# Kernel tuning notes

Measured on AMD Instinct MI355X. Metric: run time of the kernel, lower is better.

## Reference

```python
import jax, jax.numpy as jnp
import numpy as np

B, T, D, H = 4, 2048, 1024, 16
Dh = D // H

def setup_inputs() -> dict:
    key = jax.random.key(0)
    ks = jax.random.split(key, 6)
    scale = 1.0 / np.sqrt(D)
    return {
        "x": jax.random.normal(ks[0], (B, T, D), dtype=jnp.float32),
        "W_q": jax.random.normal(ks[1], (D, D), dtype=jnp.float32) * scale,
        "W_k": jax.random.normal(ks[2], (D, D), dtype=jnp.float32) * scale,
        "W_v": jax.random.normal(ks[3], (D, D), dtype=jnp.float32) * scale,
        "W_o": jax.random.normal(ks[4], (D, D), dtype=jnp.float32) * scale,
        "b_o": jax.random.normal(ks[5], (D,), dtype=jnp.float32) * 0.02,
    }

def reference(x, W_q, W_k, W_v, W_o, b_o):
    # Linear weights stored torch-style (out, in): y = x @ W.T
    def split_heads(z):
        return z.reshape(B, T, H, Dh).transpose(0, 2, 1, 3)  # [B,H,T,Dh]
    q = split_heads(x @ W_q.T)
    k = split_heads(x @ W_k.T)
    v = split_heads(x @ W_v.T)
    scale = Dh ** -0.5
    attn = jnp.einsum('bhqd,bhkd->bhqk', q, k) * scale  # [B,H,T,T]
    causal = jnp.tril(jnp.ones((T, T), dtype=bool))
    attn = jnp.where(causal[None, None], attn, -jnp.inf)
    attn = jax.nn.softmax(attn, axis=-1)
    y = jnp.einsum('bhqk,bhkd->bhqd', attn, v)  # [B,H,T,Dh]
    y = y.transpose(0, 2, 1, 3).reshape(B, T, D)
    return y @ W_o.T + b_o
```

## Files before the change

kernel.cpp:

```cpp
#include <hip/hip_runtime.h>
#include <hip/hip_bf16.h>
#include <stdint.h>

#define B_   4
#define T_   2048
#define H_   16
#define MTOT (B_ * T_)
#define NQKV 3072
#define QSC  0.18033688f

typedef __attribute__((ext_vector_type(8))) __bf16 bf16x8;
typedef __attribute__((ext_vector_type(4))) float f32x4;
typedef __attribute__((ext_vector_type(16))) float f32x16;
typedef __attribute__((ext_vector_type(4))) float f4v;
typedef __attribute__((ext_vector_type(4))) unsigned short us4;
typedef __attribute__((ext_vector_type(8))) unsigned short us8;
typedef __attribute__((ext_vector_type(4))) unsigned int u32x4;

static __device__ __forceinline__ unsigned short f2bf(float f) {
  __hip_bfloat16 h = __float2bfloat16(f);
  return __builtin_bit_cast(unsigned short, h);
}

static __device__ __forceinline__ float fast_exp2(float x) {
#if __has_builtin(__builtin_amdgcn_exp2f)
  return __builtin_amdgcn_exp2f(x);
#else
  float r; asm("v_exp_f32 %0, %1" : "=v"(r) : "v"(x)); return r;
#endif
}

static __device__ __forceinline__ void async16(const void* g, void* l) {
  __builtin_amdgcn_global_load_lds(
      (const __attribute__((address_space(1))) void*)g,
      (__attribute__((address_space(3))) void*)l, 16, 0, 0);
}

#define XHALF(res, x, OP)                                  \
  {                                                        \
    float t1_ = (x), t2_ = (x);                            \
    asm("" : "+v"(t2_));                                   \
    asm("v_permlane32_swap_b32 %0, %1" : "+v"(t1_), "+v"(t2_)); \
    res = OP(t1_, t2_);                                    \
  }
static __device__ __forceinline__ float fadd_(float a, float b) { return a + b; }

__global__ __launch_bounds__(256) void cvt_all(
    const float* __restrict__ x, const float* __restrict__ Wq,
    const float* __restrict__ Wk, const float* __restrict__ Wv,
    const float* __restrict__ Wo, unsigned short* __restrict__ xb,
    unsigned short* __restrict__ wqkv, unsigned short* __restrict__ wo) {
  int i = blockIdx.x * blockDim.x + threadIdx.x;
  const float* s; unsigned short* d; int j;
  if (i < 2097152)      { s = x;  d = xb;             j = i; }
  else if (i < 2359296) { s = Wq; d = wqkv;           j = i - 2097152; }
  else if (i < 2621440) { s = Wk; d = wqkv + 1048576; j = i - 2359296; }
  else if (i < 2883584) { s = Wv; d = wqkv + 2097152; j = i - 2621440; }
  else                  { s = Wo; d = wo;             j = i - 2883584; }
  f4v v = reinterpret_cast<const f4v*>(s)[j];
  us4 o;
  o.x = f2bf(v.x); o.y = f2bf(v.y); o.z = f2bf(v.z); o.w = f2bf(v.w);
  reinterpret_cast<us4*>(d)[j] = o;
}

template <int MODE>
__global__ __launch_bounds__(256) void gemm_bt(
    const unsigned short* __restrict__ A,
    const unsigned short* __restrict__ Bw,
    unsigned short* __restrict__ Cb,
    float* __restrict__ Cf,
    const float* __restrict__ bias,
    int K, int N) {
  __shared__ __align__(16) unsigned short As[128 * 32];
  __shared__ __align__(16) unsigned short Bs[128 * 32];

  const int t = threadIdx.x;
  const int lane = t & 63;
  const int w = t >> 6;
  const int lr = lane & 15;
  const int lg = lane >> 4;
  const int wm = w >> 1;
  const int wn = w & 1;
  const int m0 = blockIdx.y * 128;
  const int n0 = blockIdx.x * 128;

  f32x4 acc[4][4];
#pragma unroll
  for (int i = 0; i < 4; ++i)
#pragma unroll
    for (int j = 0; j < 4; ++j) acc[i][j] = (f32x4){0.f, 0.f, 0.f, 0.f};

  const int srow = t >> 2;
  const int scol = (t & 3) * 8;
  const unsigned short* ga = A + (size_t)(m0 + srow) * K + scol;
  const unsigned short* gb = Bw + (size_t)(n0 + srow) * K + scol;

  for (int k0 = 0; k0 < K; k0 += 32) {
    async16(ga + k0,                  &As[t * 8]);
    async16(ga + k0 + (size_t)64 * K, &As[2048 + t * 8]);
    async16(gb + k0,                  &Bs[t * 8]);
    async16(gb + k0 + (size_t)64 * K, &Bs[2048 + t * 8]);
    __syncthreads();

    bf16x8 af[4], bfr[4];
#pragma unroll
    for (int mi = 0; mi < 4; ++mi)
      af[mi] = *(const bf16x8*)&As[(wm * 64 + mi * 16 + lr) * 32 + lg * 8];
#pragma unroll
    for (int ni = 0; ni < 4; ++ni)
      bfr[ni] = *(const bf16x8*)&Bs[(wn * 64 + ni * 16 + lr) * 32 + lg * 8];
#pragma unroll
    for (int mi = 0; mi < 4; ++mi)
#pragma unroll
      for (int ni = 0; ni < 4; ++ni)
        acc[mi][ni] = __builtin_amdgcn_mfma_f32_16x16x32_bf16(
            af[mi], bfr[ni], acc[mi][ni], 0, 0, 0);
    __syncthreads();
  }

#pragma unroll
  for (int mi = 0; mi < 4; ++mi) {
    const int row = m0 + wm * 64 + mi * 16 + lg * 4;
#pragma unroll
    for (int ni = 0; ni < 4; ++ni) {
      const int col = n0 + wn * 64 + ni * 16 + lr;
#pragma unroll
      for (int r = 0; r < 4; ++r) {
        if (MODE == 1) {
          Cf[(size_t)(row + r) * N + col] = acc[mi][ni][r] + bias[col];
        } else {
          float v = acc[mi][ni][r];
          if (col < 1024) v *= QSC;
          Cb[(size_t)(row + r) * N + col] = f2bf(v);
        }
      }
    }
  }
}

__global__ __launch_bounds__(256, 4) void attn_kernel(
    const unsigned short* __restrict__ qkv, unsigned short* __restrict__ ob) {
  const int bid = blockIdx.x;
  const int pair = bid & 63;
  const int g = bid >> 6;
  const int rnd = g >> 2, idx = g & 3;
  const int qg = (rnd == 0) ? (15 - idx)
               : (rnd == 1) ? (8 + idx)
               : (rnd == 2) ? (7 - idx) : idx;
  const int b = pair >> 4;
  const int h = pair & 15;
  const int t = threadIdx.x;
  const int w = t >> 6;
  const int lane = t & 63;
  const int l31 = lane & 31;
  const int hi = lane >> 5;

  const int q0w = qg * 128 + w * 32;
  const int myBound = 2 * qg + (w >> 1);
  const int NT = 2 * qg + 2;

  __shared__ __align__(16) unsigned short Ks[2][64 * 64];
  __shared__ __align__(16) unsigned short Vs[2][64 * 64];

  const size_t rowbase = (size_t)(b * T_) * NQKV;

  bf16x8 Qf[4];
  {
    const unsigned short* qp =
        qkv + rowbase + (size_t)(q0w + l31) * NQKV + h * 64 + hi * 8;
#pragma unroll
    for (int m = 0; m < 4; ++m) Qf[m] = *(const bf16x8*)(qp + m * 16);
  }

  const int kr = t >> 3;
  const int ks = t & 7;
  const unsigned short* kbase =
      qkv + rowbase + 1024 + h * 64 + (ks ^ (kr & 7)) * 8 + (size_t)kr * NQKV;
  const int kvr = t >> 2;
  const int dc2 = (t & 3) * 2;
  const unsigned short* vbase =
      qkv + rowbase + 2048 + h * 64 + dc2 * 8 + (size_t)kvr * NQKV;

  float m_i = -INFINITY, l_i = 0.f;
  f32x16 o[2];
#pragma unroll
  for (int r = 0; r < 16; ++r) { o[0][r] = 0.f; o[1][r] = 0.f; }

#define VSCATTER(Vb, v0, v1)                                       \
  {                                                                \
    _Pragma("unroll") for (int i = 0; i < 8; ++i) {                \
      const int s0 = ((kvr >> 3) ^ dc2 ^ i) & 7;                   \
      const int s1 = ((kvr >> 3) ^ (dc2 + 1) ^ i) & 7;             \
      (Vb)[(dc2 * 8 + i) * 64 + s0 * 8 + (kvr & 7)] = (v0)[i];     \
      (Vb)[((dc2 + 1) * 8 + i) * 64 + s1 * 8 + (kvr & 7)] = (v1)[i]; \
    }                                                              \
  }

  {
    async16(kbase, &Ks[0][t * 8]);
    async16(kbase + (size_t)32 * NQKV, &Ks[0][2048 + t * 8]);
    us8 v0 = *(const us8*)vbase;
    us8 v1 = *(const us8*)(vbase + 8);
    VSCATTER(&Vs[0][0], v0, v1);
  }

  int cur = 0;
  for (int kt = 0; kt < NT; ++kt) {
    __syncthreads();

    const bool pf = (kt + 1 < NT);
    us8 v0, v1;
    if (pf) {
      const size_t off = (size_t)(kt + 1) * 64 * NQKV;
      async16(kbase + off, &Ks[cur ^ 1][t * 8]);
      async16(kbase + off + (size_t)32 * NQKV, &Ks[cur ^ 1][2048 + t * 8]);
      v0 = *(const us8*)(vbase + off);
      v1 = *(const us8*)(vbase + off + 8);
    }

    if (kt <= myBound) {
      const unsigned short* Kb = Ks[cur];
      const unsigned short* Vb = Vs[cur];

      f32x16 a0, a1;
#pragma unroll
      for (int r = 0; r < 16; ++r) { a0[r] = 0.f; a1[r] = 0.f; }
      {
        const int rb0 = l31 * 64;
        const int rb1 = (32 + l31) * 64;
        const int r7 = l31 & 7;
        __builtin_amdgcn_s_setprio(1);
#pragma unroll
        for (int m = 0; m < 4; ++m) {
          const int c = (((m << 1) | hi) ^ r7) * 8;
          bf16x8 kf0 = *(const bf16x8*)&Kb[rb0 + c];
          bf16x8 kf1 = *(const bf16x8*)&Kb[rb1 + c];
          a0 = __builtin_amdgcn_mfma_f32_32x32x16_bf16(kf0, Qf[m], a0, 0, 0, 0);
          a1 = __builtin_amdgcn_mfma_f32_32x32x16_bf16(kf1, Qf[m], a1, 0, 0, 0);
        }
        __builtin_amdgcn_s_setprio(0);
      }

      if (kt == myBound) {
        const int qglob = q0w + l31;
#pragma unroll
        for (int r = 0; r < 16; ++r) {
          const int kvb = kt * 64 + (r & 3) + ((r >> 2) << 3) + (hi << 2);
          if (kvb > qglob) a0[r] = -INFINITY;
          if (kvb + 32 > qglob) a1[r] = -INFINITY;
        }
      }

      float m8[8];
#pragma unroll
      for (int j = 0; j < 8; ++j)
        m8[j] = fmaxf(fmaxf(a0[j], a0[j + 8]), fmaxf(a1[j], a1[j + 8]));
      float pp = fmaxf(fmaxf(fmaxf(m8[0], m8[4]), fmaxf(m8[1], m8[5])),
                       fmaxf(fmaxf(m8[2], m8[6]), fmaxf(m8[3], m8[7])));
      float pmax;
      XHALF(pmax, pp, fmaxf);
      if (__any(pmax > m_i + 8.f)) {
        const float mnew = fmaxf(m_i, pmax);
        const float al = fast_exp2(m_i - mnew);
        m_i = mnew;
        l_i *= al;
#pragma unroll
        for (int r = 0; r < 16; ++r) { o[0][r] *= al; o[1][r] *= al; }
      }

#pragma unroll
      for (int r = 0; r < 16; ++r) {
        a0[r] = fast_exp2(a0[r] - m_i);
        a1[r] = fast_exp2(a1[r] - m_i);
      }
      float s8[8];
#pragma unroll
      for (int j = 0; j < 8; ++j)
        s8[j] = (a0[j] + a0[j + 8]) + (a1[j] + a1[j + 8]);
      float rp = ((s8[0] + s8[1]) + (s8[2] + s8[3])) +
                 ((s8[4] + s8[5]) + (s8[6] + s8[7]));
      float rs;
      XHALF(rs, rp, fadd_);
      l_i += rs;

      bf16x8 Pf[4];
#pragma unroll
      for (int m = 0; m < 4; ++m) {
        const int rb2 = (m & 1) * 8;
        uint32_t u0, u1, u2, u3;
        const f32x16& s = (m >> 1) ? a1 : a0;
        asm("v_cvt_pk_bf16_f32 %0, %1, %2" : "=v"(u0) : "v"(s[rb2 + 0]), "v"(s[rb2 + 1]));
        asm("v_cvt_pk_bf16_f32 %0, %1, %2" : "=v"(u1) : "v"(s[rb2 + 2]), "v"(s[rb2 + 3]));
        asm("v_cvt_pk_bf16_f32 %0, %1, %2" : "=v"(u2) : "v"(s[rb2 + 4]), "v"(s[rb2 + 5]));
        asm("v_cvt_pk_bf16_f32 %0, %1, %2" : "=v"(u3) : "v"(s[rb2 + 6]), "v"(s[rb2 + 7]));
        asm("v_permlane32_swap_b32 %0, %1" : "+v"(u0), "+v"(u2));
        asm("v_permlane32_swap_b32 %0, %1" : "+v"(u1), "+v"(u3));
        u32x4 pw = {u0, u1, u2, u3};
        Pf[m] = __builtin_bit_cast(bf16x8, pw);
      }

      __builtin_amdgcn_s_setprio(1);
#pragma unroll
      for (int dt = 0; dt < 2; ++dt) {
        const int d = dt * 32 + l31;
        const int base = d * 64;
        const int dsw = ((d >> 3) ^ d) & 7;
#pragma unroll
        for (int m = 0; m < 4; ++m) {
          bf16x8 vf = *(const bf16x8*)&Vb[base + ((((m << 1) | hi) ^ dsw) & 7) * 8];
          o[dt] = __builtin_amdgcn_mfma_f32_32x32x16_bf16(vf, Pf[m], o[dt], 0, 0, 0);
        }
      }
      __builtin_amdgcn_s_setprio(0);
    }

    if (pf) VSCATTER(&Vs[cur ^ 1][0], v0, v1);
    cur ^= 1;
  }

  const float rl = 1.0f / l_i;
#pragma unroll
  for (int dt = 0; dt < 2; ++dt) {
    float s[16];
#pragma unroll
    for (int r = 0; r < 16; ++r) s[r] = o[dt][r] * rl;
    uint32_t u[8];
#pragma unroll
    for (int p = 0; p < 8; ++p)
      asm("v_cvt_pk_bf16_f32 %0, %1, %2" : "=v"(u[p]) : "v"(s[2 * p]), "v"(s[2 * p + 1]));
    asm("v_permlane32_swap_b32 %0, %1" : "+v"(u[0]), "+v"(u[2]));
    asm("v_permlane32_swap_b32 %0, %1" : "+v"(u[1]), "+v"(u[3]));
    asm("v_permlane32_swap_b32 %0, %1" : "+v"(u[4]), "+v"(u[6]));
    asm("v_permlane32_swap_b32 %0, %1" : "+v"(u[5]), "+v"(u[7]));
    unsigned short* op =
        ob + (size_t)(b * T_ + q0w + l31) * 1024 + h * 64 + dt * 32 + hi * 8;
    u32x4 c0 = {u[0], u[1], u[2], u[3]};
    u32x4 c1 = {u[4], u[5], u[6], u[7]};
    *(u32x4*)op = c0;
    *(u32x4*)(op + 16) = c1;
  }
}

extern "C" void kernel_launch(void* const* d_in, const int* in_sizes, int n_in,
                              void* d_out, int out_size, void* d_ws,
                              size_t ws_size, hipStream_t stream) {
  const float* x = (const float*)d_in[0];
  const float* Wq = (const float*)d_in[1];
  const float* Wk = (const float*)d_in[2];
  const float* Wv = (const float*)d_in[3];
  const float* Wo = (const float*)d_in[4];
  const float* bo = (const float*)d_in[5];
  float* out = (float*)d_out;

  char* ws = (char*)d_ws;
  unsigned short* xb   = (unsigned short*)(ws + 0);
  unsigned short* wqkv = (unsigned short*)(ws + 16777216);
  unsigned short* wo   = (unsigned short*)(ws + 23068672);
  unsigned short* qkv  = (unsigned short*)(ws + 25165824);
  unsigned short* ob   = (unsigned short*)(ws + 75497472);
  if (ws_size < 92274688u) return;

  cvt_all<<<12288, 256, 0, stream>>>(x, Wq, Wk, Wv, Wo, xb, wqkv, wo);

  gemm_bt<0><<<dim3(NQKV / 128, MTOT / 128), 256, 0, stream>>>(
      xb, wqkv, qkv, nullptr, nullptr, 1024, NQKV);

  attn_kernel<<<dim3(1024), 256, 0, stream>>>(qkv, ob);

  gemm_bt<1><<<dim3(1024 / 128, MTOT / 128), 256, 0, stream>>>(
      ob, wo, nullptr, out, bo, 1024, 1024);
}
```

Before: 184.4 us.

## Widen GEMM K-tile to 64 with XOR-swizzled LDS and XCD-aware block mapping

The GEMM kernel now stages 64-wide K slices per iteration, which halves the number of barrier pairs. Its shared-memory layout is XOR-swizzled to avoid bank conflicts on the fragment reads. Blocks are remapped from a 1D grid so that each XCD (chosen by blockIdx & 7) gets a contiguous band of M rows, to improve L2 reuse of the A tiles. Doubling the LDS footprint may lower occupancy, and the load stage is still not overlapped with compute.

```diff
diff --git a/kernel.cpp b/kernel.cpp
--- a/kernel.cpp
+++ b/kernel.cpp
@@ -63,7 +63,7 @@
   reinterpret_cast<us4*>(d)[j] = o;
 }
 
-template <int MODE>
+template <int MODE, int NT>
 __global__ __launch_bounds__(256) void gemm_bt(
     const unsigned short* __restrict__ A,
     const unsigned short* __restrict__ Bw,
@@ -71,8 +71,14 @@
     float* __restrict__ Cf,
     const float* __restrict__ bias,
     int K, int N) {
-  __shared__ __align__(16) unsigned short As[128 * 32];
-  __shared__ __align__(16) unsigned short Bs[128 * 32];
+  __shared__ __align__(16) unsigned short As[128 * 64];
+  __shared__ __align__(16) unsigned short Bs[128 * 64];
+
+  const int bid = blockIdx.x;
+  const int xcd = bid & 7;
+  const int loc = bid >> 3;
+  const int m0 = (xcd * 8 + loc / NT) * 128;
+  const int n0 = (loc % NT) * 128;
 
   const int t = threadIdx.x;
   const int lane = t & 63;
@@ -81,8 +87,6 @@
   const int lg = lane >> 4;
   const int wm = w >> 1;
   const int wn = w & 1;
-  const int m0 = blockIdx.y * 128;
-  const int n0 = blockIdx.x * 128;
 
   f32x4 acc[4][4];
 #pragma unroll
@@ -90,31 +94,38 @@
 #pragma unroll
     for (int j = 0; j < 4; ++j) acc[i][j] = (f32x4){0.f, 0.f, 0.f, 0.f};
 
-  const int srow = t >> 2;
-  const int scol = (t & 3) * 8;
-  const unsigned short* ga = A + (size_t)(m0 + srow) * K + scol;
-  const unsigned short* gb = Bw + (size_t)(n0 + srow) * K + scol;
-
-  for (int k0 = 0; k0 < K; k0 += 32) {
-    async16(ga + k0,                  &As[t * 8]);
-    async16(ga + k0 + (size_t)64 * K, &As[2048 + t * 8]);
-    async16(gb + k0,                  &Bs[t * 8]);
-    async16(gb + k0 + (size_t)64 * K, &Bs[2048 + t * 8]);
+  const int srow = t >> 3;
+  const int gs = (t & 7) ^ ((t >> 3) & 7);
+  const unsigned short* ga = A + (size_t)(m0 + srow) * K + gs * 8;
+  const unsigned short* gb = Bw + (size_t)(n0 + srow) * K + gs * 8;
+
+  const int rsw = lr & 7;
+
+  for (int k0 = 0; k0 < K; k0 += 64) {
+#pragma unroll
+    for (int k = 0; k < 4; ++k) {
+      async16(ga + (size_t)(k * 32) * K + k0, &As[(k * 256 + t) * 8]);
+      async16(gb + (size_t)(k * 32) * K + k0, &Bs[(k * 256 + t) * 8]);
+    }
     __syncthreads();
 
-    bf16x8 af[4], bfr[4];
-#pragma unroll
-    for (int mi = 0; mi < 4; ++mi)
-      af[mi] = *(const bf16x8*)&As[(wm * 64 + mi * 16 + lr) * 32 + lg * 8];
-#pragma unroll
-    for (int ni = 0; ni < 4; ++ni)
-      bfr[ni] = *(const bf16x8*)&Bs[(wn * 64 + ni * 16 + lr) * 32 + lg * 8];
-#pragma unroll
-    for (int mi = 0; mi < 4; ++mi)
+#pragma unroll
+    for (int kk = 0; kk < 2; ++kk) {
+      const int slot = ((kk * 4 + lg) ^ rsw) * 8;
+      bf16x8 af[4], bfr[4];
+#pragma unroll
+      for (int mi = 0; mi < 4; ++mi)
+        af[mi] = *(const bf16x8*)&As[(wm * 64 + mi * 16 + lr) * 64 + slot];
 #pragma unroll
       for (int ni = 0; ni < 4; ++ni)
-        acc[mi][ni] = __builtin_amdgcn_mfma_f32_16x16x32_bf16(
-            af[mi], bfr[ni], acc[mi][ni], 0, 0, 0);
+        bfr[ni] = *(const bf16x8*)&Bs[(wn * 64 + ni * 16 + lr) * 64 + slot];
+#pragma unroll
+      for (int mi = 0; mi < 4; ++mi)
+#pragma unroll
+        for (int ni = 0; ni < 4; ++ni)
+          acc[mi][ni] = __builtin_amdgcn_mfma_f32_16x16x32_bf16(
+              af[mi], bfr[ni], acc[mi][ni], 0, 0, 0);
+    }
     __syncthreads();
   }
 
@@ -362,11 +373,11 @@
 
   cvt_all<<<12288, 256, 0, stream>>>(x, Wq, Wk, Wv, Wo, xb, wqkv, wo);
 
-  gemm_bt<0><<<dim3(NQKV / 128, MTOT / 128), 256, 0, stream>>>(
+  gemm_bt<0, 24><<<1536, 256, 0, stream>>>(
       xb, wqkv, qkv, nullptr, nullptr, 1024, NQKV);
 
   attn_kernel<<<dim3(1024), 256, 0, stream>>>(qkv, ob);
 
-  gemm_bt<1><<<dim3(1024 / 128, MTOT / 128), 256, 0, stream>>>(
+  gemm_bt<1, 8><<<512, 256, 0, stream>>>(
       ob, wo, nullptr, out, bo, 1024, 1024);
 }
```

Result: faster. 170.5 us (-7.5%).
